# Performance work log

Measured on AMD Instinct MI355X. Metric: run time of the kernel, lower is better.

## Reference

```python
import jax, jax.numpy as jnp
import numpy as np

NU, NV = 8192, 8192
IN_DIM, HID, NCLS = 128, 64, 5


def setup_inputs() -> dict:
    key = jax.random.key(0)
    k1, k2, k3, k4, k5, k6, k7 = jax.random.split(key, 7)
    return {
        "u": jax.random.normal(k1, (NU, IN_DIM), dtype=jnp.float32),
        "v": jax.random.normal(k2, (NV, IN_DIM), dtype=jnp.float32),
        "adj": jax.random.uniform(k3, (NU, NV), dtype=jnp.float32),
        "degree": jax.random.uniform(k4, (NU + NV,), dtype=jnp.float32),
        "u_weight": jax.random.normal(k5, (NCLS, IN_DIM, HID), dtype=jnp.float32),
        "v_weight": jax.random.normal(k6, (NCLS, IN_DIM, HID), dtype=jnp.float32),
        "bias": jax.random.normal(k7, (HID,), dtype=jnp.float32),
        "r": 4,
    }


def reference(u, v, adj, degree, u_weight, v_weight, bias, r):
    # Sum weight slices for rating classes 0..r (r is a static Python int).
    Wu = jnp.sum(u_weight[: r + 1], axis=0)  # [IN_DIM, HID]
    Wv = jnp.sum(v_weight[: r + 1], axis=0)
    # Dropout is identity at p=0.0 (eval mode).
    su = u @ Wu  # [NU, HID]
    sv = v @ Wv  # [NV, HID]
    nu = adj.shape[0]
    # Block adjacency [[0, A], [A^T, 0]] row-scaled by diag(degree), applied to
    # concat(su, sv) -- computed block-wise, same math without the dense block matrix.
    top = degree[:nu, None] * (adj @ sv)      # [NU, HID]
    bot = degree[nu:, None] * (adj.T @ su)    # [NV, HID]
    return jnp.concatenate([top, bot], axis=0) + bias
```

## Files before the change

### kernel.cpp

```cpp
#include <hip/hip_runtime.h>
#include <stdint.h>


#define HID 64
#define IN_DIM 128
#define NROWS 8192
#define NCLS 5

typedef float f32x4 __attribute__((ext_vector_type(4)));
typedef short s16x8 __attribute__((ext_vector_type(8)));
typedef short s16x4 __attribute__((ext_vector_type(4)));
typedef unsigned short u16;

#define PACK_SIDE 524288

static __device__ __forceinline__ short f2b(float x) {
    unsigned u = __builtin_bit_cast(unsigned, x);
    return (short)((u + 0x7FFFu + ((u >> 16) & 1u)) >> 16);
}

__global__ __launch_bounds__(256, 2) void k_prep(
    const float* __restrict__ u, const float* __restrict__ v,
    const float* __restrict__ uw, const float* __restrict__ vw,
    const int* __restrict__ rp, u16* __restrict__ ws)
{
    __shared__ float W[IN_DIM * HID];
    __shared__ float X[64 * 129];

    const int y = blockIdx.y;
    const float* __restrict__ src  = y ? v  : u;
    const float* __restrict__ wsrc = y ? vw : uw;
    u16* __restrict__ dstP = ws + (size_t)y * PACK_SIDE;
    const int i0 = blockIdx.x * 64;
    const int t = threadIdx.x;
    int r = *rp; if (r > NCLS - 1) r = NCLS - 1; if (r < 0) r = 0;

    for (int idx = t; idx < IN_DIM * HID; idx += 256) {
        float s = 0.f;
        for (int c = 0; c <= r; ++c) s += wsrc[c * (IN_DIM * HID) + idx];
        W[idx] = s;
    }
    #pragma unroll
    for (int qq = 0; qq < 8; ++qq) {
        int idx = t + qq * 256;
        int row = idx >> 5, c4 = idx & 31;
        f32x4 val = *(const f32x4*)&src[(size_t)(i0 + row) * IN_DIM + c4 * 4];
        float* d = &X[row * 129 + c4 * 4];
        d[0] = val[0]; d[1] = val[1]; d[2] = val[2]; d[3] = val[3];
    }
    __syncthreads();

    const int i = t & 63, h0 = (t >> 6) * 16;
    float acc[16];
    #pragma unroll
    for (int k = 0; k < 16; ++k) acc[k] = 0.f;
    for (int c = 0; c < IN_DIM; ++c) {
        float uv = X[i * 129 + c];
        const f32x4* wr = (const f32x4*)&W[c * HID + h0];
        f32x4 w0 = wr[0], w1 = wr[1], w2 = wr[2], w3 = wr[3];
        acc[0]  += uv * w0[0]; acc[1]  += uv * w0[1];
        acc[2]  += uv * w0[2]; acc[3]  += uv * w0[3];
        acc[4]  += uv * w1[0]; acc[5]  += uv * w1[1];
        acc[6]  += uv * w1[2]; acc[7]  += uv * w1[3];
        acc[8]  += uv * w2[0]; acc[9]  += uv * w2[1];
        acc[10] += uv * w2[2]; acc[11] += uv * w2[3];
        acc[12] += uv * w3[0]; acc[13] += uv * w3[1];
        acc[14] += uv * w3[2]; acc[15] += uv * w3[3];
    }
    const int iL = i0 + i;
    u16* __restrict__ dp = dstP
        + (((size_t)(iL >> 5) * 4 + (h0 >> 4)) << 9)
        + ((iL >> 3) & 3) * 128
        + (iL & 7);
    #pragma unroll
    for (int hh = 0; hh < 16; ++hh)
        dp[hh * 8] = (u16)f2b(acc[hh]);
}

__global__ __launch_bounds__(256, 2) void k_main(
    const float* __restrict__ adj, const u16* __restrict__ ws,
    float* __restrict__ wst, float* __restrict__ wsb)
{
    __shared__ u16 P[64][256];

    const int bx = blockIdx.x;
    const int R0 = (bx >> 5) * 256, C0 = (bx & 31) * 256;
    const int t = threadIdx.x;
    const int w = t >> 6, l = t & 63;
    const int q = l >> 4, l15 = l & 15;
    const u16* __restrict__ BPl_u = ws + (size_t)l * 8;
    const u16* __restrict__ BPl_v = ws + PACK_SIDE + (size_t)l * 8;

    f32x4 accB[8][4];
    #pragma unroll
    for (int mt = 0; mt < 8; ++mt)
        #pragma unroll
        for (int nn = 0; nn < 4; ++nn) accB[mt][nn] = (f32x4){0.f, 0.f, 0.f, 0.f};

    for (int p = 0; p < 4; ++p) {
        {
            const float* __restrict__ src =
                adj + (size_t)(R0 + p * 64 + w * 16) * NROWS + C0 + l * 4;
            #pragma unroll
            for (int rr = 0; rr < 16; rr += 4) {
                f32x4 d0 = *(const f32x4*)(src + (size_t)(rr + 0) * NROWS);
                f32x4 d1 = *(const f32x4*)(src + (size_t)(rr + 1) * NROWS);
                f32x4 d2 = *(const f32x4*)(src + (size_t)(rr + 2) * NROWS);
                f32x4 d3 = *(const f32x4*)(src + (size_t)(rr + 3) * NROWS);
                #pragma unroll
                for (int i = 0; i < 4; ++i) {
                    f32x4 d = (i == 0) ? d0 : (i == 1) ? d1 : (i == 2) ? d2 : d3;
                    const int row = w * 16 + rr + i;
                    s16x4 b;
                    b[0] = f2b(d[0]); b[1] = f2b(d[1]);
                    b[2] = f2b(d[2]); b[3] = f2b(d[3]);
                    *(s16x4*)&P[row][(((l >> 1) ^ (row & 7)) << 3) + ((l & 1) << 2)] = b;
                }
            }
        }
        __syncthreads();

        if (w < 2) {
            f32x4 accT[2][4];
            #pragma unroll
            for (int mt = 0; mt < 2; ++mt)
                #pragma unroll
                for (int nn = 0; nn < 4; ++nn) accT[mt][nn] = (f32x4){0.f, 0.f, 0.f, 0.f};
            #pragma unroll
            for (int kk = 0; kk < 8; ++kk) {
                const int kb = (C0 >> 5) + kk;
                s16x8 bf[4];
                #pragma unroll
                for (int nn = 0; nn < 4; ++nn)
                    bf[nn] = *(const s16x8*)(BPl_v + ((size_t)(kb * 4 + nn) << 9));
                #pragma unroll
                for (int mt = 0; mt < 2; ++mt) {
                    const int row = w * 32 + mt * 16 + l15;
                    s16x8 af = *(const s16x8*)&P[row][((kk * 4 + q) ^ (row & 7)) << 3];
                    #pragma unroll
                    for (int nn = 0; nn < 4; ++nn)
                        accT[mt][nn] = __builtin_amdgcn_mfma_f32_16x16x32_bf16(
                            af, bf[nn], accT[mt][nn], 0, 0, 0);
                }
            }
            float* __restrict__ WT = wst + (size_t)(bx & 31) * (NROWS * HID)
                                   + (size_t)(R0 + p * 64 + w * 32) * HID;
            #pragma unroll
            for (int mt = 0; mt < 2; ++mt)
                #pragma unroll
                for (int nn = 0; nn < 4; ++nn)
                    #pragma unroll
                    for (int rg = 0; rg < 4; ++rg)
                        WT[(size_t)(mt * 16 + q * 4 + rg) * HID + nn * 16 + l15] =
                            accT[mt][nn][rg];
        } else {
            #pragma unroll
            for (int kk = 0; kk < 2; ++kk) {
                const int kb = (R0 >> 5) + p * 2 + kk;
                s16x8 bf[4];
                #pragma unroll
                for (int nn = 0; nn < 4; ++nn)
                    bf[nn] = *(const s16x8*)(BPl_u + ((size_t)(kb * 4 + nn) << 9));
                #pragma unroll
                for (int mt = 0; mt < 8; ++mt) {
                    const int j = (w - 2) * 128 + mt * 16 + l15;
                    s16x8 af;
                    #pragma unroll
                    for (int tt = 0; tt < 8; ++tt) {
                        const int row = kk * 32 + q * 8 + tt;
                        af[tt] = (short)P[row][(((j >> 3) ^ tt) << 3) + (j & 7)];
                    }
                    #pragma unroll
                    for (int nn = 0; nn < 4; ++nn)
                        accB[mt][nn] = __builtin_amdgcn_mfma_f32_16x16x32_bf16(
                            af, bf[nn], accB[mt][nn], 0, 0, 0);
                }
            }
        }
        __syncthreads();
    }

    if (w >= 2) {
        float* __restrict__ WB = wsb + (size_t)(bx >> 5) * (NROWS * HID)
                               + (size_t)(C0 + (w - 2) * 128) * HID;
        #pragma unroll
        for (int mt = 0; mt < 8; ++mt)
            #pragma unroll
            for (int nn = 0; nn < 4; ++nn)
                #pragma unroll
                for (int rg = 0; rg < 4; ++rg)
                    WB[(size_t)(mt * 16 + q * 4 + rg) * HID + nn * 16 + l15] =
                        accB[mt][nn][rg];
    }
}

__global__ __launch_bounds__(256, 4) void k_fin(
    const float* __restrict__ degree, const float* __restrict__ bias,
    const float* __restrict__ wst, const float* __restrict__ wsb,
    float* __restrict__ out)
{
    const int b = blockIdx.x;
    const int side = (b >= 512);
    const int t = threadIdx.x;
    const int r = (b & 511) * 16 + (t >> 4);
    const int c4 = (t & 15) * 4;
    const float* __restrict__ W = side ? wsb : wst;

    f32x4 s = (f32x4){0.f, 0.f, 0.f, 0.f};
    #pragma unroll
    for (int c = 0; c < 32; ++c)
        s += *(const f32x4*)&W[(size_t)c * (NROWS * HID) + (size_t)r * HID + c4];
    const int grow = side * NROWS + r;
    const float d = degree[grow];
    f32x4 bb = *(const f32x4*)&bias[c4];
    *(f32x4*)&out[(size_t)grow * HID + c4] = d * s + bb;
}

extern "C" void kernel_launch(void* const* d_in, const int* in_sizes, int n_in,
                              void* d_out, int out_size, void* d_ws, size_t ws_size,
                              hipStream_t stream) {
    (void)in_sizes; (void)n_in; (void)out_size; (void)ws_size;
    const float* u      = (const float*)d_in[0];
    const float* v      = (const float*)d_in[1];
    const float* adj    = (const float*)d_in[2];
    const float* degree = (const float*)d_in[3];
    const float* uw     = (const float*)d_in[4];
    const float* vw     = (const float*)d_in[5];
    const float* bias   = (const float*)d_in[6];
    const int*   rp     = (const int*)d_in[7];
    u16*   ws  = (u16*)d_ws;
    float* wst = (float*)(ws + 2 * PACK_SIDE);
    float* wsb = wst + (size_t)32 * NROWS * HID;
    float* out = (float*)d_out;

    k_prep<<<dim3(128, 2), 256, 0, stream>>>(u, v, uw, vw, rp, ws);
    k_main<<<dim3(1024),   256, 0, stream>>>(adj, ws, wst, wsb);
    k_fin <<<dim3(1024),   256, 0, stream>>>(degree, bias, wst, wsb, out);
}
```

Baseline: 529.8 us.

## Double-buffer adjacency tiles in LDS and prefetch next chunk into registers

The main kernel now processes the 256-row tile in eight 32-row chunks, not four 64-row chunks. Two LDS buffers alternate so each iteration needs one barrier instead of two. The next chunk's global loads are issued into registers before the MFMA work on the current chunk, so memory latency overlaps compute. The cost is more loop iterations with smaller MFMA work per phase, plus hand-placed waitcnt and barrier intrinsics that bypass the compiler's synchronization.

```diff
diff --git a/kernel.cpp b/kernel.cpp
--- a/kernel.cpp
+++ b/kernel.cpp
@@ -81,7 +81,7 @@
     const float* __restrict__ adj, const u16* __restrict__ ws,
     float* __restrict__ wst, float* __restrict__ wsb)
 {
-    __shared__ u16 P[64][256];
+    __shared__ u16 P[2][32 * 256];
 
     const int bx = blockIdx.x;
     const int R0 = (bx >> 5) * 256, C0 = (bx & 31) * 256;
@@ -90,6 +90,7 @@
     const int q = l >> 4, l15 = l & 15;
     const u16* __restrict__ BPl_u = ws + (size_t)l * 8;
     const u16* __restrict__ BPl_v = ws + PACK_SIDE + (size_t)l * 8;
+    const float* __restrict__ apw = adj + (size_t)(R0 + w * 8) * NROWS + C0 + l * 4;
 
     f32x4 accB[8][4];
     #pragma unroll
@@ -97,35 +98,38 @@
         #pragma unroll
         for (int nn = 0; nn < 4; ++nn) accB[mt][nn] = (f32x4){0.f, 0.f, 0.f, 0.f};
 
-    for (int p = 0; p < 4; ++p) {
-        {
-            const float* __restrict__ src =
-                adj + (size_t)(R0 + p * 64 + w * 16) * NROWS + C0 + l * 4;
-            #pragma unroll
-            for (int rr = 0; rr < 16; rr += 4) {
-                f32x4 d0 = *(const f32x4*)(src + (size_t)(rr + 0) * NROWS);
-                f32x4 d1 = *(const f32x4*)(src + (size_t)(rr + 1) * NROWS);
-                f32x4 d2 = *(const f32x4*)(src + (size_t)(rr + 2) * NROWS);
-                f32x4 d3 = *(const f32x4*)(src + (size_t)(rr + 3) * NROWS);
-                #pragma unroll
-                for (int i = 0; i < 4; ++i) {
-                    f32x4 d = (i == 0) ? d0 : (i == 1) ? d1 : (i == 2) ? d2 : d3;
-                    const int row = w * 16 + rr + i;
-                    s16x4 b;
-                    b[0] = f2b(d[0]); b[1] = f2b(d[1]);
-                    b[2] = f2b(d[2]); b[3] = f2b(d[3]);
-                    *(s16x4*)&P[row][(((l >> 1) ^ (row & 7)) << 3) + ((l & 1) << 2)] = b;
-                }
-            }
+    f32x4 reg[8];
+    #pragma unroll
+    for (int rr = 0; rr < 8; ++rr)
+        reg[rr] = *(const f32x4*)(apw + (size_t)rr * NROWS);
+
+    for (int p = 0; p < 8; ++p) {
+        u16* __restrict__ Pb = P[p & 1];
+
+        #pragma unroll
+        for (int rr = 0; rr < 8; ++rr) {
+            const int row = w * 8 + rr;
+            s16x4 b;
+            b[0] = f2b(reg[rr][0]); b[1] = f2b(reg[rr][1]);
+            b[2] = f2b(reg[rr][2]); b[3] = f2b(reg[rr][3]);
+            *(s16x4*)&Pb[row * 256 + (((l >> 1) ^ rr) << 3) + ((l & 1) << 2)] = b;
         }
-        __syncthreads();
+
+        if (p < 7) {
+            #pragma unroll
+            for (int rr = 0; rr < 8; ++rr)
+                reg[rr] = *(const f32x4*)(apw + (size_t)((p + 1) * 32 + rr) * NROWS);
+        }
+
+        asm volatile("s_waitcnt lgkmcnt(0)" ::: "memory");
+        __builtin_amdgcn_s_barrier();
+        __builtin_amdgcn_sched_barrier(0);
 
         if (w < 2) {
-            f32x4 accT[2][4];
-            #pragma unroll
-            for (int mt = 0; mt < 2; ++mt)
-                #pragma unroll
-                for (int nn = 0; nn < 4; ++nn) accT[mt][nn] = (f32x4){0.f, 0.f, 0.f, 0.f};
+            f32x4 accT[4];
+            #pragma unroll
+            for (int nn = 0; nn < 4; ++nn) accT[nn] = (f32x4){0.f, 0.f, 0.f, 0.f};
+            const int rp = w * 16 + l15;
             #pragma unroll
             for (int kk = 0; kk < 8; ++kk) {
                 const int kb = (C0 >> 5) + kk;
@@ -133,51 +137,38 @@
                 #pragma unroll
                 for (int nn = 0; nn < 4; ++nn)
                     bf[nn] = *(const s16x8*)(BPl_v + ((size_t)(kb * 4 + nn) << 9));
-                #pragma unroll
-                for (int mt = 0; mt < 2; ++mt) {
-                    const int row = w * 32 + mt * 16 + l15;
-                    s16x8 af = *(const s16x8*)&P[row][((kk * 4 + q) ^ (row & 7)) << 3];
-                    #pragma unroll
-                    for (int nn = 0; nn < 4; ++nn)
-                        accT[mt][nn] = __builtin_amdgcn_mfma_f32_16x16x32_bf16(
-                            af, bf[nn], accT[mt][nn], 0, 0, 0);
-                }
+                s16x8 af = *(const s16x8*)&Pb[rp * 256 + (((kk * 4 + q) ^ (rp & 7)) << 3)];
+                #pragma unroll
+                for (int nn = 0; nn < 4; ++nn)
+                    accT[nn] = __builtin_amdgcn_mfma_f32_16x16x32_bf16(
+                        af, bf[nn], accT[nn], 0, 0, 0);
             }
             float* __restrict__ WT = wst + (size_t)(bx & 31) * (NROWS * HID)
-                                   + (size_t)(R0 + p * 64 + w * 32) * HID;
-            #pragma unroll
-            for (int mt = 0; mt < 2; ++mt)
+                                   + (size_t)(R0 + p * 32 + w * 16) * HID;
+            #pragma unroll
+            for (int nn = 0; nn < 4; ++nn)
+                #pragma unroll
+                for (int rg = 0; rg < 4; ++rg)
+                    WT[(size_t)(q * 4 + rg) * HID + nn * 16 + l15] = accT[nn][rg];
+        } else {
+            const int kb = (R0 >> 5) + p;
+            s16x8 bf[4];
+            #pragma unroll
+            for (int nn = 0; nn < 4; ++nn)
+                bf[nn] = *(const s16x8*)(BPl_u + ((size_t)(kb * 4 + nn) << 9));
+            #pragma unroll
+            for (int mt = 0; mt < 8; ++mt) {
+                const int j = (w - 2) * 128 + mt * 16 + l15;
+                s16x8 af;
+                #pragma unroll
+                for (int tt = 0; tt < 8; ++tt)
+                    af[tt] = (short)Pb[(q * 8 + tt) * 256 + (((j >> 3) ^ tt) << 3) + (j & 7)];
                 #pragma unroll
                 for (int nn = 0; nn < 4; ++nn)
-                    #pragma unroll
-                    for (int rg = 0; rg < 4; ++rg)
-                        WT[(size_t)(mt * 16 + q * 4 + rg) * HID + nn * 16 + l15] =
-                            accT[mt][nn][rg];
-        } else {
-            #pragma unroll
-            for (int kk = 0; kk < 2; ++kk) {
-                const int kb = (R0 >> 5) + p * 2 + kk;
-                s16x8 bf[4];
-                #pragma unroll
-                for (int nn = 0; nn < 4; ++nn)
-                    bf[nn] = *(const s16x8*)(BPl_u + ((size_t)(kb * 4 + nn) << 9));
-                #pragma unroll
-                for (int mt = 0; mt < 8; ++mt) {
-                    const int j = (w - 2) * 128 + mt * 16 + l15;
-                    s16x8 af;
-                    #pragma unroll
-                    for (int tt = 0; tt < 8; ++tt) {
-                        const int row = kk * 32 + q * 8 + tt;
-                        af[tt] = (short)P[row][(((j >> 3) ^ tt) << 3) + (j & 7)];
-                    }
-                    #pragma unroll
-                    for (int nn = 0; nn < 4; ++nn)
-                        accB[mt][nn] = __builtin_amdgcn_mfma_f32_16x16x32_bf16(
-                            af, bf[nn], accB[mt][nn], 0, 0, 0);
-                }
+                    accB[mt][nn] = __builtin_amdgcn_mfma_f32_16x16x32_bf16(
+                        af, bf[nn], accB[mt][nn], 0, 0, 0);
             }
         }
-        __syncthreads();
     }
 
     if (w >= 2) {
```

After: 551.5 us. +4.1%, slower.
